# Kernel optimization log

Hardware: AMD Instinct MI355X
Metric: run time of the kernel (lower is better)

Reference implementation:

```python
import jax, jax.numpy as jnp
import numpy as np

# Model dims
B, S, D = 2, 1024, 1024          # batch, seq, d_model
NH, HD = 16, 64                  # n_heads, head_dim
E, K, H = 8, 2, 4096             # num_experts, experts_per_token, expert hidden
EPS = 1e-6
ROPE_BASE = 10000.0


def rmsnorm(x, w):
    # RMSNorm: x * rsqrt(mean(x^2) + eps) * weight (no mean-centering, no bias)
    return x * jax.lax.rsqrt(jnp.mean(x * x, axis=-1, keepdims=True) + EPS) * w


def apply_rope(q, k):
    # q,k: [B, NH, S, HD]; position_ids = arange(S) broadcast over batch
    hd = q.shape[-1]
    s = q.shape[2]
    inv_freq = 1.0 / (ROPE_BASE ** (jnp.arange(0, hd, 2, dtype=jnp.float32) / hd))
    freqs = jnp.arange(s, dtype=jnp.float32)[:, None] * inv_freq          # [S, HD/2]
    emb = jnp.concatenate([freqs, freqs], axis=-1)                        # [S, HD]
    cos = jnp.cos(emb)[None, None]                                        # [1,1,S,HD]
    sin = jnp.sin(emb)[None, None]

    def rotate_half(x):
        x1, x2 = jnp.split(x, 2, axis=-1)
        return jnp.concatenate([-x2, x1], axis=-1)

    return q * cos + rotate_half(q) * sin, k * cos + rotate_half(k) * sin


def setup_inputs() -> dict:
    key = jax.random.key(0)
    ks = jax.random.split(key, 9)
    sc = 0.02
    return {
        "x": jax.random.normal(ks[0], (B, S, D), jnp.float32),
        "attn_norm_w": jnp.ones((D,), jnp.float32),
        "wq": jax.random.normal(ks[1], (D, D), jnp.float32) * sc,
        "wk": jax.random.normal(ks[2], (D, D), jnp.float32) * sc,
        "wv": jax.random.normal(ks[3], (D, D), jnp.float32) * sc,
        "wo": jax.random.normal(ks[4], (D, D), jnp.float32) * sc,
        "moe_norm_w": jnp.ones((D,), jnp.float32),
        "gate_w": jax.random.normal(ks[5], (E, D), jnp.float32) * sc,
        "w1": jax.random.normal(ks[6], (E, H, D), jnp.float32) * sc,
        "b1": jnp.zeros((E, H), jnp.float32),
        "w2": jax.random.normal(ks[7], (E, D, H), jnp.float32) * sc,
        "b2": jnp.zeros((E, D), jnp.float32),
    }


def reference(x, attn_norm_w, wq, wk, wv, wo, moe_norm_w, gate_w, w1, b1, w2, b2):
    b, s, d = x.shape
    # --- pre-norm causal self-attention with RoPE (eval mode: no dropout) ---
    t = rmsnorm(x, attn_norm_w)
    q = (t @ wq.T).reshape(b, s, NH, HD).transpose(0, 2, 1, 3)
    k = (t @ wk.T).reshape(b, s, NH, HD).transpose(0, 2, 1, 3)
    v = (t @ wv.T).reshape(b, s, NH, HD).transpose(0, 2, 1, 3)
    q, k = apply_rope(q, k)
    scores = jnp.einsum("bhqd,bhkd->bhqk", q, k) / np.float32(np.sqrt(HD))
    causal = jnp.tril(jnp.ones((s, s), bool))
    scores = jnp.where(causal, scores, jnp.float32(-1e30))
    attn = jax.nn.softmax(scores, axis=-1)
    ao = jnp.einsum("bhqk,bhkd->bhqd", attn, v).transpose(0, 2, 1, 3).reshape(b, s, d)
    h = x + ao @ wo.T

    # --- sparse top-k MoE FFN (internal RMSNorm + residual) ---
    tn = rmsnorm(h, moe_norm_w).reshape(-1, d)                  # [T, D]
    logits = tn @ gate_w.T                                      # [T, E]
    gate_scores, idx = jax.lax.top_k(logits, K)                 # [T, K]
    rw = jax.nn.softmax(gate_scores, axis=-1)                   # [T, K]
    # compute all experts densely, then gather selected (same math as
    # gathering per-token expert weight matrices, far less memory traffic)
    hid = jax.nn.gelu(jnp.einsum("td,ehd->teh", tn, w1) + b1, approximate=False)
    eo = jnp.einsum("teh,edh->ted", hid, w2) + b2               # [T, E, D]
    sel = jnp.take_along_axis(eo, idx[:, :, None], axis=1)      # [T, K, D]
    moe_out = jnp.einsum("tkd,tk->td", sel, rw).reshape(b, s, d)
    return h + moe_out
```

## Files before the change

kernel.cpp:

```cpp
#include <hip/hip_runtime.h>
#include <hip/hip_bf16.h>
#include <hip/hip_fp16.h>


#define T_TOK 2048
#define DMODEL 1024
#define SEQ 1024
#define NEXP 8
#define HEXP 4096

typedef __attribute__((ext_vector_type(4))) float f32x4;
typedef __attribute__((ext_vector_type(4))) int i32x4;
typedef __attribute__((ext_vector_type(8))) short short8;
typedef __attribute__((ext_vector_type(8))) _Float16 half8;
typedef __attribute__((ext_vector_type(4))) _Float16 half4;

#define WAIT_VM3 asm volatile("s_waitcnt vmcnt(3)" ::: "memory")
#define WAIT_VM4 asm volatile("s_waitcnt vmcnt(4)" ::: "memory")
#define WAIT_VM6 asm volatile("s_waitcnt vmcnt(6)" ::: "memory")
#define WAIT_VM0 asm volatile("s_waitcnt vmcnt(0)" ::: "memory")
#define BARRIER __builtin_amdgcn_s_barrier()
#define SCHEDFENCE __builtin_amdgcn_sched_barrier(0)

__device__ __forceinline__ void gload16(const void* g, void* l)
{
    __builtin_amdgcn_global_load_lds((const __attribute__((address_space(1))) void*)g,
                                     (__attribute__((address_space(3))) void*)l, 16, 0, 0);
}

__device__ __forceinline__ void bsplit(float f, unsigned short& hi, unsigned short& lo)
{
    unsigned int u = __float_as_uint(f);
    unsigned int rh = (u + 0x7FFFu + ((u >> 16) & 1u)) >> 16;
    hi = (unsigned short)rh;
    float fl = f - __uint_as_float(rh << 16);
    unsigned int u2 = __float_as_uint(fl);
    lo = (unsigned short)((u2 + 0x7FFFu + ((u2 >> 16) & 1u)) >> 16);
}

__device__ __forceinline__ float gelu_fast(float v)
{
    float e = __expf(-1.5957691216f * v * (1.0f + 0.044715f * v * v));
    return v * __builtin_amdgcn_rcpf(1.0f + e);
}

__global__ __launch_bounds__(256) void cast2_f16_kernel(
    const float* __restrict__ s0, const float* __restrict__ s1,
    _Float16* __restrict__ d0, _Float16* __restrict__ d1, int n16)
{
    const float* src = blockIdx.y ? s1 : s0;
    _Float16* dst = blockIdx.y ? d1 : d0;
    int stride = gridDim.x * blockDim.x;
    for (int i = blockIdx.x * blockDim.x + threadIdx.x; i < n16; i += stride) {
        float4 a = ((const float4*)src)[4 * i];
        float4 b = ((const float4*)src)[4 * i + 1];
        float4 c = ((const float4*)src)[4 * i + 2];
        float4 d = ((const float4*)src)[4 * i + 3];
        half8 h0 = { (_Float16)a.x, (_Float16)a.y, (_Float16)a.z, (_Float16)a.w,
                     (_Float16)b.x, (_Float16)b.y, (_Float16)b.z, (_Float16)b.w };
        half8 h1 = { (_Float16)c.x, (_Float16)c.y, (_Float16)c.z, (_Float16)c.w,
                     (_Float16)d.x, (_Float16)d.y, (_Float16)d.z, (_Float16)d.w };
        *(half8*)(dst + (size_t)i * 16) = h0;
        *(half8*)(dst + (size_t)i * 16 + 8) = h1;
    }
}

__global__ __launch_bounds__(256) void split4_kernel(
    const float* __restrict__ s0, const float* __restrict__ s1,
    const float* __restrict__ s2, const float* __restrict__ s3,
    unsigned short* __restrict__ h0, unsigned short* __restrict__ h1,
    unsigned short* __restrict__ h2, unsigned short* __restrict__ h3,
    unsigned short* __restrict__ l0, unsigned short* __restrict__ l1,
    unsigned short* __restrict__ l2, unsigned short* __restrict__ l3, int n4)
{
    int z = blockIdx.y;
    const float* src = (z == 0) ? s0 : (z == 1) ? s1 : (z == 2) ? s2 : s3;
    unsigned short* hi = (z == 0) ? h0 : (z == 1) ? h1 : (z == 2) ? h2 : h3;
    unsigned short* lo = (z == 0) ? l0 : (z == 1) ? l1 : (z == 2) ? l2 : l3;
    int stride = gridDim.x * blockDim.x;
    for (int i = blockIdx.x * blockDim.x + threadIdx.x; i < n4; i += stride) {
        float4 v = ((const float4*)src)[i];
        ushort4 h, l;
        bsplit(v.x, h.x, l.x); bsplit(v.y, h.y, l.y);
        bsplit(v.z, h.z, l.z); bsplit(v.w, h.w, l.w);
        *(ushort4*)(hi + (size_t)i * 4) = h;
        *(ushort4*)(lo + (size_t)i * 4) = l;
    }
}

__global__ __launch_bounds__(256) void rmsnorm_kernel(const float* __restrict__ x,
                                                      const float* __restrict__ w,
                                                      float* __restrict__ of,
                                                      _Float16* __restrict__ oh,
                                                      unsigned short* __restrict__ ohi,
                                                      unsigned short* __restrict__ olo)
{
    int row = blockIdx.x;
    int t = threadIdx.x;
    float4 v = ((const float4*)(x + (size_t)row * DMODEL))[t];
    float ss = v.x * v.x + v.y * v.y + v.z * v.z + v.w * v.w;
#pragma unroll
    for (int off = 32; off > 0; off >>= 1) ss += __shfl_xor(ss, off);
    __shared__ float red[4];
    if ((t & 63) == 0) red[t >> 6] = ss;
    __syncthreads();
    float tot = red[0] + red[1] + red[2] + red[3];
    float sc = rsqrtf(tot * (1.0f / DMODEL) + 1e-6f);
    float4 w4 = ((const float4*)w)[t];
    float4 o;
    o.x = v.x * sc * w4.x; o.y = v.y * sc * w4.y; o.z = v.z * sc * w4.z; o.w = v.w * sc * w4.w;
    if (of) ((float4*)(of + (size_t)row * DMODEL))[t] = o;
    if (oh) {
        half4 h = { (_Float16)o.x, (_Float16)o.y, (_Float16)o.z, (_Float16)o.w };
        *(half4*)(oh + (size_t)row * DMODEL + t * 4) = h;
    }
    if (ohi) {
        ushort4 h, l;
        bsplit(o.x, h.x, l.x); bsplit(o.y, h.y, l.y);
        bsplit(o.z, h.z, l.z); bsplit(o.w, h.w, l.w);
        *(ushort4*)(ohi + (size_t)row * DMODEL + t * 4) = h;
        *(ushort4*)(olo + (size_t)row * DMODEL + t * 4) = l;
    }
}

__global__ __launch_bounds__(256) void gemm_split_kernel(
    const unsigned short* __restrict__ aH, const unsigned short* __restrict__ aL,
    const unsigned short* __restrict__ b0H, const unsigned short* __restrict__ b0L,
    const unsigned short* __restrict__ b1H, const unsigned short* __restrict__ b1L,
    const unsigned short* __restrict__ b2H, const unsigned short* __restrict__ b2L,
    float* __restrict__ C0, float* __restrict__ C1, float* __restrict__ C2,
    const float* __restrict__ resid, int K)
{
    const unsigned short* bH = (blockIdx.z == 0) ? b0H : (blockIdx.z == 1 ? b1H : b2H);
    const unsigned short* bL = (blockIdx.z == 0) ? b0L : (blockIdx.z == 1 ? b1L : b2L);
    float* C = (blockIdx.z == 0) ? C0 : (blockIdx.z == 1 ? C1 : C2);
    int m0 = blockIdx.y * 128, n0 = blockIdx.x * 64;
    __shared__ unsigned short AsH[2][128 * 32];
    __shared__ unsigned short AsL[2][128 * 32];
    __shared__ unsigned short BsH[2][64 * 32];
    __shared__ unsigned short BsL[2][64 * 32];
    int t = threadIdx.x, w = t >> 6, l = t & 63;
    int sa = l >> 2, sc = (l & 3) * 8;
    const unsigned short* gAH0 = aH + (size_t)(m0 + w * 32 + sa) * K + sc;
    const unsigned short* gAH1 = aH + (size_t)(m0 + w * 32 + 16 + sa) * K + sc;
    const unsigned short* gAL0 = aL + (size_t)(m0 + w * 32 + sa) * K + sc;
    const unsigned short* gAL1 = aL + (size_t)(m0 + w * 32 + 16 + sa) * K + sc;
    const unsigned short* gBH0 = bH + (size_t)(n0 + w * 16 + sa) * K + sc;
    const unsigned short* gBL0 = bL + (size_t)(n0 + w * 16 + sa) * K + sc;
    const int aoff0 = (w * 32) * 32;
    const int aoff1 = (w * 32 + 16) * 32;
    const int boff0 = (w * 16) * 32;
    int wr = w >> 1, wc = w & 1;
    f32x4 zero = { 0.0f, 0.0f, 0.0f, 0.0f };
    f32x4 acc[4][2];
#pragma unroll
    for (int i = 0; i < 4; i++)
#pragma unroll
        for (int j = 0; j < 2; j++) acc[i][j] = zero;

#define GS_STAGE(B, K0) do { \
    gload16(gAH0 + (K0), &AsH[B][aoff0]); gload16(gAH1 + (K0), &AsH[B][aoff1]); \
    gload16(gAL0 + (K0), &AsL[B][aoff0]); gload16(gAL1 + (K0), &AsL[B][aoff1]); \
    gload16(gBH0 + (K0), &BsH[B][boff0]); gload16(gBL0 + (K0), &BsL[B][boff0]); \
} while (0)

#define GS_COMPUTE(B) do { \
    short8 ah[4], al[4], bh8[2], bl8[2]; \
    _Pragma("unroll") \
    for (int mi = 0; mi < 4; mi++) { \
        int base = (wr * 64 + mi * 16 + (l & 15)) * 32 + (l >> 4) * 8; \
        ah[mi] = *(const short8*)&AsH[B][base]; \
        al[mi] = *(const short8*)&AsL[B][base]; } \
    _Pragma("unroll") \
    for (int ni = 0; ni < 2; ni++) { \
        int base = (wc * 32 + ni * 16 + (l & 15)) * 32 + (l >> 4) * 8; \
        bh8[ni] = *(const short8*)&BsH[B][base]; \
        bl8[ni] = *(const short8*)&BsL[B][base]; } \
    _Pragma("unroll") \
    for (int mi = 0; mi < 4; mi++) \
        _Pragma("unroll") \
        for (int ni = 0; ni < 2; ni++) { \
            acc[mi][ni] = __builtin_amdgcn_mfma_f32_16x16x32_bf16(ah[mi], bh8[ni], acc[mi][ni], 0, 0, 0); \
            acc[mi][ni] = __builtin_amdgcn_mfma_f32_16x16x32_bf16(ah[mi], bl8[ni], acc[mi][ni], 0, 0, 0); \
            acc[mi][ni] = __builtin_amdgcn_mfma_f32_16x16x32_bf16(al[mi], bh8[ni], acc[mi][ni], 0, 0, 0); } \
} while (0)

    const int nt = K >> 5;
    GS_STAGE(0, 0);
    for (int kt = 0; kt < nt; kt += 2) {
        GS_STAGE(1, (kt + 1) << 5);
        WAIT_VM6;
        BARRIER; SCHEDFENCE;
        GS_COMPUTE(0);
        BARRIER;
        if (kt + 2 < nt) {
            GS_STAGE(0, (kt + 2) << 5);
            WAIT_VM6;
        } else {
            WAIT_VM0;
        }
        BARRIER; SCHEDFENCE;
        GS_COMPUTE(1);
        BARRIER;
    }
#undef GS_STAGE
#undef GS_COMPUTE

#pragma unroll
    for (int mi = 0; mi < 4; mi++) {
#pragma unroll
        for (int r = 0; r < 4; r++) {
            int row = m0 + wr * 64 + mi * 16 + (l >> 4) * 4 + r;
#pragma unroll
            for (int ni = 0; ni < 2; ni++) {
                int col = n0 + wc * 32 + ni * 16 + (l & 15);
                float v = acc[mi][ni][r];
                if (resid) v += resid[(size_t)row * DMODEL + col];
                C[(size_t)row * DMODEL + col] = v;
            }
        }
    }
}

__global__ __launch_bounds__(256) void rope_split_kernel(
    const float* __restrict__ qf, const float* __restrict__ kf,
    unsigned short* __restrict__ qHi, unsigned short* __restrict__ qLo,
    unsigned short* __restrict__ kHi, unsigned short* __restrict__ kLo)
{
    int i = blockIdx.x * 256 + threadIdx.x;
    int tok = i >> 9;
    int r = i & 511;
    int hh = r >> 5, ii = r & 31;
    int s = tok & (SEQ - 1);
    int b = tok >> 10;
    float invf = powf(10000.0f, -(float)(2 * ii) * (1.0f / 64.0f));
    float ang = (float)s * invf;
    float c = cosf(ang), sn = sinf(ang);
    size_t base = (size_t)tok * DMODEL + hh * 64 + ii;
    float q1 = qf[base], q2 = qf[base + 32];
    float k1 = kf[base], k2 = kf[base + 32];
    float rq1 = (q1 * c - q2 * sn) * 0.125f;
    float rq2 = (q2 * c + q1 * sn) * 0.125f;
    float rk1 = k1 * c - k2 * sn;
    float rk2 = k2 * c + k1 * sn;
    int bh = b * 16 + hh;
    size_t qb = ((size_t)bh * SEQ + s) * 64 + ii;
    unsigned short h, lo;
    bsplit(rq1, h, lo); qHi[qb] = h; qLo[qb] = lo;
    bsplit(rq2, h, lo); qHi[qb + 32] = h; qLo[qb + 32] = lo;
    size_t kb = (size_t)bh * (SEQ * 64) + (size_t)(s >> 6) * 4096 + (size_t)(s & 63) * 64;
    int d1 = ii, d2 = ii + 32;
    int p1 = (((d1 >> 3) ^ (s & 7)) << 3) | (d1 & 7);
    int p2 = (((d2 >> 3) ^ (s & 7)) << 3) | (d2 & 7);
    bsplit(rk1, h, lo); kHi[kb + p1] = h; kLo[kb + p1] = lo;
    bsplit(rk2, h, lo); kHi[kb + p2] = h; kLo[kb + p2] = lo;
}

__global__ __launch_bounds__(256) void vtrans_kernel(const float* __restrict__ vf,
                                                     unsigned short* __restrict__ vtHi,
                                                     unsigned short* __restrict__ vtLo)
{
    int sb = blockIdx.x, bh = blockIdx.y;
    int b = bh >> 4, h = bh & 15;
    __shared__ unsigned short tH[64][72];
    __shared__ unsigned short tL[64][72];
    int t = threadIdx.x;
#pragma unroll
    for (int i = 0; i < 4; i++) {
        int idx = i * 256 + t, row = idx >> 4, c4 = idx & 15;
        float4 v = *(const float4*)(vf + (size_t)(b * SEQ + sb * 64 + row) * DMODEL + h * 64 + c4 * 4);
        unsigned short hh, ll;
        bsplit(v.x, hh, ll); tH[c4 * 4 + 0][row] = hh; tL[c4 * 4 + 0][row] = ll;
        bsplit(v.y, hh, ll); tH[c4 * 4 + 1][row] = hh; tL[c4 * 4 + 1][row] = ll;
        bsplit(v.z, hh, ll); tH[c4 * 4 + 2][row] = hh; tL[c4 * 4 + 2][row] = ll;
        bsplit(v.w, hh, ll); tH[c4 * 4 + 3][row] = hh; tL[c4 * 4 + 3][row] = ll;
    }
    __syncthreads();
#pragma unroll
    for (int i = 0; i < 4; i++) {
        int idx = i * 256 + t, d = idx >> 4, sc4 = idx & 15;
        ushort4 oh = { tH[d][sc4 * 4 + 0], tH[d][sc4 * 4 + 1], tH[d][sc4 * 4 + 2], tH[d][sc4 * 4 + 3] };
        ushort4 ol = { tL[d][sc4 * 4 + 0], tL[d][sc4 * 4 + 1], tL[d][sc4 * 4 + 2], tL[d][sc4 * 4 + 3] };
        size_t off = (size_t)bh * (64 * SEQ) + (size_t)sb * 4096 + (size_t)d * 64
                   + (((sc4 >> 1) ^ (d & 7)) << 3) + ((sc4 & 1) << 2);
        *(ushort4*)(vtHi + off) = oh;
        *(ushort4*)(vtLo + off) = ol;
    }
}

__global__ __launch_bounds__(512) void attn_mfma_kernel(
    const unsigned short* __restrict__ qHi, const unsigned short* __restrict__ qLo,
    const unsigned short* __restrict__ kHi, const unsigned short* __restrict__ kLo,
    const unsigned short* __restrict__ vtHi, const unsigned short* __restrict__ vtLo,
    float* __restrict__ Opart, float* __restrict__ mscr, float* __restrict__ lscr)
{
    int qt = 7 - blockIdx.x;
    int bh = blockIdx.y, ks = blockIdx.z;
    int t = threadIdx.x, w = t >> 6, l = t & 63;
    int lq = l & 15, g = l >> 4, lx = lq & 7;
    __shared__ unsigned short KsH[2][4096];
    __shared__ unsigned short KsL[2][4096];
    __shared__ unsigned short VsH[2][4096];
    __shared__ unsigned short VsL[2][4096];
    __shared__ unsigned short PsH[8][1024];
    __shared__ unsigned short PsL[8][1024];
    const size_t hb = (size_t)bh * (SEQ * 64);
    const unsigned short* kHp = kHi + hb;
    const unsigned short* kLp = kLo + hb;
    const unsigned short* vHp = vtHi + hb;
    const unsigned short* vLp = vtLo + hb;
    int qrow = qt * 128 + w * 16 + lq;
    short8 qh[2], qlo8[2];
#pragma unroll
    for (int c = 0; c < 2; c++) {
        size_t off = hb + (size_t)qrow * 64 + c * 32 + g * 8;
        qh[c]   = *(const short8*)(qHi + off);
        qlo8[c] = *(const short8*)(qLo + off);
    }
    f32x4 zero = { 0.0f, 0.0f, 0.0f, 0.0f };
    f32x4 acc_o[4];
#pragma unroll
    for (int i = 0; i < 4; i++) acc_o[i] = zero;
    float mrun = -3.0e38f, lrun = 0.0f;
    int ktl = ks ? (qt + 1) : 0;
    int kth = ks ? (2 * qt + 2) : (qt + 1);

#define AT_STAGE(B, KT) do { \
    size_t so = (size_t)(KT) * 4096 + (w * 64 + l) * 8; \
    gload16(kHp + so, &KsH[B][w * 512]); \
    gload16(kLp + so, &KsL[B][w * 512]); \
    gload16(vHp + so, &VsH[B][w * 512]); \
    gload16(vLp + so, &VsL[B][w * 512]); \
} while (0)

#define AT_COMPUTE(B, KT) do { \
    f32x4 sacc[4]; \
    _Pragma("unroll") \
    for (int i = 0; i < 4; i++) sacc[i] = zero; \
    _Pragma("unroll") \
    for (int nf = 0; nf < 4; nf++) { \
        _Pragma("unroll") \
        for (int c = 0; c < 2; c++) { \
            int ka = (nf * 16 + lq) * 64 + (((c * 4 + g) ^ lx) << 3); \
            short8 kh = *(const short8*)&KsH[B][ka]; \
            short8 kl = *(const short8*)&KsL[B][ka]; \
            sacc[nf] = __builtin_amdgcn_mfma_f32_16x16x32_bf16(kh, qh[c], sacc[nf], 0, 0, 0); \
            sacc[nf] = __builtin_amdgcn_mfma_f32_16x16x32_bf16(kh, qlo8[c], sacc[nf], 0, 0, 0); \
            sacc[nf] = __builtin_amdgcn_mfma_f32_16x16x32_bf16(kl, qh[c], sacc[nf], 0, 0, 0); \
        } \
    } \
    _Pragma("unroll") \
    for (int nf = 0; nf < 4; nf++) \
        _Pragma("unroll") \
        for (int r = 0; r < 4; r++) \
            if ((KT) * 64 + nf * 16 + g * 4 + r > qrow) sacc[nf][r] = -1.0e30f; \
    float mt = sacc[0][0]; \
    _Pragma("unroll") \
    for (int nf = 0; nf < 4; nf++) \
        _Pragma("unroll") \
        for (int r = 0; r < 4; r++) mt = fmaxf(mt, sacc[nf][r]); \
    mt = fmaxf(mt, __shfl_xor(mt, 16)); \
    mt = fmaxf(mt, __shfl_xor(mt, 32)); \
    float mnew = fmaxf(mrun, mt); \
    float p[4][4]; \
    float ps = 0.0f; \
    _Pragma("unroll") \
    for (int nf = 0; nf < 4; nf++) \
        _Pragma("unroll") \
        for (int r = 0; r < 4; r++) { \
            float e = __expf(sacc[nf][r] - mnew); \
            p[nf][r] = e; \
            ps += e; \
        } \
    ps += __shfl_xor(ps, 16); \
    ps += __shfl_xor(ps, 32); \
    float scale = __expf(mrun - mnew); \
    lrun = lrun * scale + ps; \
    mrun = mnew; \
    _Pragma("unroll") \
    for (int nf = 0; nf < 4; nf++) { \
        ushort4 ph, pl; \
        bsplit(p[nf][0], ph.x, pl.x); bsplit(p[nf][1], ph.y, pl.y); \
        bsplit(p[nf][2], ph.z, pl.z); bsplit(p[nf][3], ph.w, pl.w); \
        int pa = lq * 64 + (((nf * 2 + (g >> 1)) ^ lx) << 3) + ((g & 1) << 2); \
        *(ushort4*)&PsH[w][pa] = ph; \
        *(ushort4*)&PsL[w][pa] = pl; \
    } \
    float scq[4]; \
    _Pragma("unroll") \
    for (int r = 0; r < 4; r++) scq[r] = __shfl(scale, g * 4 + r); \
    _Pragma("unroll") \
    for (int df = 0; df < 4; df++) \
        _Pragma("unroll") \
        for (int r = 0; r < 4; r++) acc_o[df][r] *= scq[r]; \
    _Pragma("unroll") \
    for (int c = 0; c < 2; c++) { \
        int pa = lq * 64 + (((c * 4 + g) ^ lx) << 3); \
        short8 ph8 = *(const short8*)&PsH[w][pa]; \
        short8 pl8 = *(const short8*)&PsL[w][pa]; \
        _Pragma("unroll") \
        for (int df = 0; df < 4; df++) { \
            int va = (df * 16 + lq) * 64 + (((c * 4 + g) ^ lx) << 3); \
            short8 vh = *(const short8*)&VsH[B][va]; \
            short8 vl = *(const short8*)&VsL[B][va]; \
            acc_o[df] = __builtin_amdgcn_mfma_f32_16x16x32_bf16(ph8, vh, acc_o[df], 0, 0, 0); \
            acc_o[df] = __builtin_amdgcn_mfma_f32_16x16x32_bf16(ph8, vl, acc_o[df], 0, 0, 0); \
            acc_o[df] = __builtin_amdgcn_mfma_f32_16x16x32_bf16(pl8, vh, acc_o[df], 0, 0, 0); \
        } \
    } \
} while (0)

    int kt = ktl;
    AT_STAGE(0, kt);
    for (; kt + 1 < kth; kt += 2) {
        AT_STAGE(1, kt + 1);
        WAIT_VM4;
        BARRIER; SCHEDFENCE;
        AT_COMPUTE(0, kt);
        BARRIER;
        if (kt + 2 < kth) {
            AT_STAGE(0, kt + 2);
            WAIT_VM4;
        } else {
            WAIT_VM0;
        }
        BARRIER; SCHEDFENCE;
        AT_COMPUTE(1, kt + 1);
        BARRIER;
    }
    if (kt < kth) {
        WAIT_VM0;
        BARRIER; SCHEDFENCE;
        AT_COMPUTE(0, kt);
    }
#undef AT_STAGE
#undef AT_COMPUTE

    if (g == 0) {
        size_t mi = (size_t)(ks * 32 + bh) * SEQ + (size_t)(qt * 128 + w * 16 + lq);
        mscr[mi] = mrun;
        lscr[mi] = lrun;
    }
#pragma unroll
    for (int df = 0; df < 4; df++)
#pragma unroll
        for (int r = 0; r < 4; r++) {
            size_t row = (size_t)(ks * 32 + bh) * SEQ + (size_t)(qt * 128 + w * 16 + g * 4 + r);
            Opart[row * 64 + df * 16 + lq] = acc_o[df][r];
        }
}

__global__ __launch_bounds__(256) void attn_combine_kernel(
    const float* __restrict__ Opart, const float* __restrict__ mscr,
    const float* __restrict__ lscr,
    unsigned short* __restrict__ aoHi, unsigned short* __restrict__ aoLo)
{
    int i = blockIdx.x * 256 + threadIdx.x;
    int d4 = i & 15;
    int qr = (i >> 4) & (SEQ - 1);
    int bh = i >> 14;
    int b = bh >> 4, h = bh & 15;
    size_t r0 = (size_t)bh * SEQ + qr;
    size_t r1 = (size_t)(32 + bh) * SEQ + qr;
    float m0 = mscr[r0], m1 = mscr[r1];
    float l0 = lscr[r0], l1 = lscr[r1];
    float m = fmaxf(m0, m1);
    float w0 = __expf(m0 - m), w1 = __expf(m1 - m);
    float dn = 1.0f / (w0 * l0 + w1 * l1);
    float4 o0 = *(const float4*)(Opart + r0 * 64 + d4 * 4);
    float4 o1 = *(const float4*)(Opart + r1 * 64 + d4 * 4);
    float4 o;
    o.x = (w0 * o0.x + w1 * o1.x) * dn;
    o.y = (w0 * o0.y + w1 * o1.y) * dn;
    o.z = (w0 * o0.z + w1 * o1.z) * dn;
    o.w = (w0 * o0.w + w1 * o1.w) * dn;
    ushort4 hs, ls;
    bsplit(o.x, hs.x, ls.x); bsplit(o.y, hs.y, ls.y);
    bsplit(o.z, hs.z, ls.z); bsplit(o.w, hs.w, ls.w);
    size_t base = (size_t)b * SEQ * DMODEL + (size_t)qr * DMODEL + h * 64 + d4 * 4;
    *(ushort4*)(aoHi + base) = hs;
    *(ushort4*)(aoLo + base) = ls;
}

__global__ __launch_bounds__(256) void gate_kernel(const float* __restrict__ tn2f,
                                                   const float* __restrict__ gw,
                                                   float* __restrict__ logits)
{
    int tok = blockIdx.x;
    int t = threadIdx.x, e = t >> 5, l32 = t & 31;
    const float* xr = tn2f + (size_t)tok * DMODEL;
    const float* gr = gw + (size_t)e * DMODEL;
    float s = 0.0f;
    for (int j = l32; j < DMODEL; j += 32) s += xr[j] * gr[j];
#pragma unroll
    for (int off = 16; off > 0; off >>= 1) s += __shfl_down(s, off, 32);
    if (l32 == 0) logits[tok * NEXP + e] = s;
}

__global__ void zero_kernel(int* p, int n)
{
    int i = blockIdx.x * blockDim.x + threadIdx.x;
    if (i < n) p[i] = 0;
}

__global__ void top2_kernel(const float* __restrict__ logits, float* __restrict__ rw,
                            int* __restrict__ cnt, int* __restrict__ entry)
{
    int t = blockIdx.x * blockDim.x + threadIdx.x;
    if (t >= T_TOK) return;
    float l[8];
#pragma unroll
    for (int e = 0; e < 8; e++) l[e] = logits[t * 8 + e];
    int e0 = 0;
#pragma unroll
    for (int e = 1; e < 8; e++) if (l[e] > l[e0]) e0 = e;
    int e1 = (e0 == 0) ? 1 : 0;
#pragma unroll
    for (int e = 0; e < 8; e++) if (e != e0 && l[e] > l[e1]) e1 = e;
    float ex = expf(l[e1] - l[e0]);
    float denom = 1.0f + ex;
    rw[t * 2 + 0] = 1.0f / denom;
    rw[t * 2 + 1] = ex / denom;
    int pos = atomicAdd(&cnt[e0], 1);
    entry[e0 * 2048 + pos] = t * 2;
    pos = atomicAdd(&cnt[e1], 1);
    entry[e1 * 2048 + pos] = t * 2 + 1;
}

__global__ void offs_kernel(const int* __restrict__ cnt, int* __restrict__ offs)
{
    if (threadIdx.x == 0) {
        int s = 0;
        for (int e = 0; e < 8; e++) { offs[e] = s; s += cnt[e]; }
    }
}

__global__ __launch_bounds__(256) void moe_gemm1_kernel(
    const _Float16* __restrict__ tn2h, const _Float16* __restrict__ w1h,
    const float* __restrict__ b1, const int* __restrict__ cnt, const int* __restrict__ offs,
    const int* __restrict__ entry, _Float16* __restrict__ hid)
{
    int bid = blockIdx.x;
    int e = bid & 7;
    int n_i = (bid >> 3) & 31;
    int m_i = bid >> 8;
    int ne = cnt[e];
    int m0 = m_i * 128;
    if (m0 >= ne) return;
    int n0 = n_i * 128;
    __shared__ _Float16 As[2][128 * 32];
    __shared__ _Float16 Bs[2][128 * 32];
    int t = threadIdx.x, w = t >> 6, l = t & 63;
    int sa = l >> 2, sc = (l & 3) * 8;
    int g0 = entry[e * 2048 + min(m0 + w * 32 + sa, ne - 1)] >> 1;
    int g1 = entry[e * 2048 + min(m0 + w * 32 + 16 + sa, ne - 1)] >> 1;
    const _Float16* gA0 = tn2h + (size_t)g0 * DMODEL + sc;
    const _Float16* gA1 = tn2h + (size_t)g1 * DMODEL + sc;
    const _Float16* w1e = w1h + (size_t)e * HEXP * DMODEL;
    const _Float16* gB0 = w1e + (size_t)(n0 + w * 32 + sa) * DMODEL + sc;
    const _Float16* gB1 = w1e + (size_t)(n0 + w * 32 + 16 + sa) * DMODEL + sc;
    const int aoff0 = (w * 32) * 32, aoff1 = (w * 32 + 16) * 32;
    int wr = w >> 1, wc = w & 1;
    f32x4 zero = { 0.0f, 0.0f, 0.0f, 0.0f };
    f32x4 acc[4][4];
#pragma unroll
    for (int i = 0; i < 4; i++)
#pragma unroll
        for (int j = 0; j < 4; j++) acc[i][j] = zero;

#define M1_STAGE(B, K0) do { \
    gload16(gA0 + (K0), &As[B][aoff0]); gload16(gA1 + (K0), &As[B][aoff1]); \
    gload16(gB0 + (K0), &Bs[B][aoff0]); gload16(gB1 + (K0), &Bs[B][aoff1]); \
} while (0)

#define M1_COMPUTE(B) do { \
    half8 af[4], bfr[4]; \
    _Pragma("unroll") \
    for (int mi = 0; mi < 4; mi++) \
        af[mi] = *(const half8*)&As[B][(wr * 64 + mi * 16 + (l & 15)) * 32 + (l >> 4) * 8]; \
    _Pragma("unroll") \
    for (int ni = 0; ni < 4; ni++) \
        bfr[ni] = *(const half8*)&Bs[B][(wc * 64 + ni * 16 + (l & 15)) * 32 + (l >> 4) * 8]; \
    _Pragma("unroll") \
    for (int mi = 0; mi < 4; mi++) \
        _Pragma("unroll") \
        for (int ni = 0; ni < 4; ni++) \
            acc[mi][ni] = __builtin_amdgcn_mfma_f32_16x16x32_f16(af[mi], bfr[ni], acc[mi][ni], 0, 0, 0); \
} while (0)

    const int nt = DMODEL >> 5;
    M1_STAGE(0, 0);
    for (int kt = 0; kt < nt; kt += 2) {
        M1_STAGE(1, (kt + 1) << 5);
        WAIT_VM4;
        BARRIER; SCHEDFENCE;
        M1_COMPUTE(0);
        BARRIER;
        if (kt + 2 < nt) {
            M1_STAGE(0, (kt + 2) << 5);
            WAIT_VM4;
        } else {
            WAIT_VM0;
        }
        BARRIER; SCHEDFENCE;
        M1_COMPUTE(1);
        BARRIER;
    }
#undef M1_STAGE
#undef M1_COMPUTE

    int off_e = offs[e];
#pragma unroll
    for (int mi = 0; mi < 4; mi++) {
#pragma unroll
        for (int r = 0; r < 4; r++) {
            int row = m0 + wr * 64 + mi * 16 + (l >> 4) * 4 + r;
            if (row < ne) {
                size_t orow = (size_t)(off_e + row) * HEXP;
#pragma unroll
                for (int ni = 0; ni < 4; ni++) {
                    int cg = n0 + wc * 64 + ni * 16 + (l & 15);
                    float v = acc[mi][ni][r] + b1[e * HEXP + cg];
                    hid[orow + cg] = (_Float16)gelu_fast(v);
                }
            }
        }
    }
}

__global__ __launch_bounds__(512) void moe_gemm2_kernel(
    const _Float16* __restrict__ hid, const _Float16* __restrict__ w2h,
    const float* __restrict__ b2, const int* __restrict__ cnt, const int* __restrict__ offs,
    const int* __restrict__ entry,
    float* __restrict__ eoA, float* __restrict__ eoB,
    float* __restrict__ eoC, float* __restrict__ eoD)
{
    int bid = blockIdx.x;
    int e = bid & 7;
    int rest = bid >> 3;
    int n_i = rest & 7;
    int rest2 = rest >> 3;
    int ks = rest2 & 3;
    int m_i = rest2 >> 2;
    int ne = cnt[e];
    int m0 = m_i * 256;
    if (m0 >= ne) return;
    int n0 = n_i * 128;
    int kbase = ks * (HEXP / 4);
    float* eoP = (ks == 0) ? eoA : (ks == 1) ? eoB : (ks == 2) ? eoC : eoD;
    __shared__ _Float16 As[2][256 * 32];
    __shared__ _Float16 Bs[2][128 * 32];
    int t = threadIdx.x, w = t >> 6, l = t & 63;
    int off_e = offs[e];
    int sa = l >> 2, sc = (l & 3) * 8;
    int r0 = off_e + min(m0 + w * 32 + sa, ne - 1);
    int r1 = off_e + min(m0 + w * 32 + 16 + sa, ne - 1);
    const _Float16* gA0 = hid + (size_t)r0 * HEXP + kbase + sc;
    const _Float16* gA1 = hid + (size_t)r1 * HEXP + kbase + sc;
    const _Float16* w2e = w2h + (size_t)e * DMODEL * HEXP;
    const _Float16* gB0 = w2e + (size_t)(n0 + w * 16 + sa) * HEXP + kbase + sc;
    const int aoff0 = (w * 32) * 32, aoff1 = (w * 32 + 16) * 32;
    const int boff0 = (w * 16) * 32;
    int wr = w >> 1, wc = w & 1;
    f32x4 zero = { 0.0f, 0.0f, 0.0f, 0.0f };
    f32x4 acc[4][4];
#pragma unroll
    for (int i = 0; i < 4; i++)
#pragma unroll
        for (int j = 0; j < 4; j++) acc[i][j] = zero;

#define M2_STAGE(B, K0) do { \
    gload16(gA0 + (K0), &As[B][aoff0]); gload16(gA1 + (K0), &As[B][aoff1]); \
    gload16(gB0 + (K0), &Bs[B][boff0]); \
} while (0)

#define M2_COMPUTE(B) do { \
    half8 af[4], bfr[4]; \
    _Pragma("unroll") \
    for (int mi = 0; mi < 4; mi++) \
        af[mi] = *(const half8*)&As[B][(wr * 64 + mi * 16 + (l & 15)) * 32 + (l >> 4) * 8]; \
    _Pragma("unroll") \
    for (int ni = 0; ni < 4; ni++) \
        bfr[ni] = *(const half8*)&Bs[B][(wc * 64 + ni * 16 + (l & 15)) * 32 + (l >> 4) * 8]; \
    _Pragma("unroll") \
    for (int mi = 0; mi < 4; mi++) \
        _Pragma("unroll") \
        for (int ni = 0; ni < 4; ni++) \
            acc[mi][ni] = __builtin_amdgcn_mfma_f32_16x16x32_f16(af[mi], bfr[ni], acc[mi][ni], 0, 0, 0); \
} while (0)

    const int nt = (HEXP / 4) >> 5;
    M2_STAGE(0, 0);
    for (int kt = 0; kt < nt; kt += 2) {
        M2_STAGE(1, (kt + 1) << 5);
        WAIT_VM3;
        BARRIER; SCHEDFENCE;
        M2_COMPUTE(0);
        BARRIER;
        if (kt + 2 < nt) {
            M2_STAGE(0, (kt + 2) << 5);
            WAIT_VM3;
        } else {
            WAIT_VM0;
        }
        BARRIER; SCHEDFENCE;
        M2_COMPUTE(1);
        BARRIER;
    }
#undef M2_STAGE
#undef M2_COMPUTE

#pragma unroll
    for (int mi = 0; mi < 4; mi++) {
#pragma unroll
        for (int r = 0; r < 4; r++) {
            int row = m0 + wr * 64 + mi * 16 + (l >> 4) * 4 + r;
            if (row < ne) {
                int t2k = entry[e * 2048 + row];
#pragma unroll
                for (int ni = 0; ni < 4; ni++) {
                    int cg = n0 + wc * 64 + ni * 16 + (l & 15);
                    float v = acc[mi][ni][r];
                    if (ks == 0) v += b2[e * DMODEL + cg];
                    eoP[(size_t)t2k * DMODEL + cg] = v;
                }
            }
        }
    }
}

__global__ __launch_bounds__(256) void combine_kernel(const float* __restrict__ hf,
                                                      const float* __restrict__ eoA,
                                                      const float* __restrict__ eoB,
                                                      const float* __restrict__ eoC,
                                                      const float* __restrict__ eoD,
                                                      const float* __restrict__ rw,
                                                      float* __restrict__ out)
{
    int i = blockIdx.x * 256 + threadIdx.x;
    int tok = i >> 8;
    int d4 = i & 255;
    float4 hv = ((const float4*)hf)[i];
    float p0 = rw[tok * 2], p1 = rw[tok * 2 + 1];
    size_t i0 = (size_t)(tok * 2) * 256 + d4;
    size_t i1 = (size_t)(tok * 2 + 1) * 256 + d4;
    float4 a0 = ((const float4*)eoA)[i0];
    float4 b0 = ((const float4*)eoB)[i0];
    float4 c0 = ((const float4*)eoC)[i0];
    float4 d0 = ((const float4*)eoD)[i0];
    float4 a1 = ((const float4*)eoA)[i1];
    float4 b1 = ((const float4*)eoB)[i1];
    float4 c1 = ((const float4*)eoC)[i1];
    float4 d1 = ((const float4*)eoD)[i1];
    float4 o;
    o.x = hv.x + p0 * (a0.x + b0.x + c0.x + d0.x) + p1 * (a1.x + b1.x + c1.x + d1.x);
    o.y = hv.y + p0 * (a0.y + b0.y + c0.y + d0.y) + p1 * (a1.y + b1.y + c1.y + d1.y);
    o.z = hv.z + p0 * (a0.z + b0.z + c0.z + d0.z) + p1 * (a1.z + b1.z + c1.z + d1.z);
    o.w = hv.w + p0 * (a0.w + b0.w + c0.w + d0.w) + p1 * (a1.w + b1.w + c1.w + d1.w);
    ((float4*)out)[i] = o;
}

extern "C" void kernel_launch(void* const* d_in, const int* in_sizes, int n_in,
                              void* d_out, int out_size, void* d_ws, size_t ws_size,
                              hipStream_t stream)
{
    const float* x   = (const float*)d_in[0];
    const float* anw = (const float*)d_in[1];
    const float* wq  = (const float*)d_in[2];
    const float* wk  = (const float*)d_in[3];
    const float* wv  = (const float*)d_in[4];
    const float* wo  = (const float*)d_in[5];
    const float* mnw = (const float*)d_in[6];
    const float* gw  = (const float*)d_in[7];
    const float* w1  = (const float*)d_in[8];
    const float* b1  = (const float*)d_in[9];
    const float* w2  = (const float*)d_in[10];
    const float* b2  = (const float*)d_in[11];
    float* out = (float*)d_out;

    char* p = (char*)d_ws;
    auto alloc = [&](size_t bytes) { char* q = p; p += (bytes + 255) & ~(size_t)255; return q; };
    const size_t TD = (size_t)T_TOK * DMODEL;
    unsigned short* tnHi = (unsigned short*)alloc(TD * 2);
    unsigned short* tnLo = (unsigned short*)alloc(TD * 2);
    float*    qf   = (float*)alloc(TD * 4);
    float*    kf   = (float*)alloc(TD * 4);
    float*    vf   = (float*)alloc(TD * 4);
    unsigned short* qHi = (unsigned short*)alloc(TD * 2);
    unsigned short* qLo = (unsigned short*)alloc(TD * 2);
    unsigned short* kHi = (unsigned short*)alloc(TD * 2);
    unsigned short* kLo = (unsigned short*)alloc(TD * 2);
    float*    hf   = (float*)alloc(TD * 4);
    unsigned short* wqH = (unsigned short*)alloc((size_t)DMODEL * DMODEL * 2);
    unsigned short* wqL = (unsigned short*)alloc((size_t)DMODEL * DMODEL * 2);
    unsigned short* wkH = (unsigned short*)alloc((size_t)DMODEL * DMODEL * 2);
    unsigned short* wkL = (unsigned short*)alloc((size_t)DMODEL * DMODEL * 2);
    unsigned short* wvH = (unsigned short*)alloc((size_t)DMODEL * DMODEL * 2);
    unsigned short* wvL = (unsigned short*)alloc((size_t)DMODEL * DMODEL * 2);
    unsigned short* woH = (unsigned short*)alloc((size_t)DMODEL * DMODEL * 2);
    unsigned short* woL = (unsigned short*)alloc((size_t)DMODEL * DMODEL * 2);
    _Float16* w1h  = (_Float16*)alloc((size_t)NEXP * HEXP * DMODEL * 2);
    _Float16* w2h  = (_Float16*)alloc((size_t)NEXP * HEXP * DMODEL * 2);
    _Float16* hid  = (_Float16*)alloc((size_t)4096 * HEXP * 2);
    float*    logits = (float*)alloc((size_t)T_TOK * NEXP * 4);
    float*    rw   = (float*)alloc((size_t)T_TOK * 2 * 4);
    int*      cnt  = (int*)alloc(256);
    int*      offs = (int*)alloc(256);
    int*      entry = (int*)alloc((size_t)NEXP * 2048 * 4);
    float*    mscr = (float*)alloc((size_t)2 * 32 * SEQ * 4);
    float*    lscr = (float*)alloc((size_t)2 * 32 * SEQ * 4);
    (void)ws_size; (void)in_sizes; (void)n_in; (void)out_size;

    unsigned short* vtHi = (unsigned short*)qf;
    unsigned short* vtLo = (unsigned short*)qf + TD;
    float* tn2f = qf;
    unsigned short* aoHi = (unsigned short*)kf;
    unsigned short* aoLo = (unsigned short*)kf + TD;
    _Float16* tn2h = (_Float16*)vf;
    float* eoA = (float*)qHi;
    float* eoB = (float*)wqH;
    float* Opart = (float*)w1h;
    float* eoC = (float*)((char*)w1h + (size_t)32 * 1024 * 1024);
    float* eoD = (float*)((char*)w1h + (size_t)48 * 1024 * 1024);

    split4_kernel<<<dim3(512, 4), 256, 0, stream>>>(wq, wk, wv, wo,
        wqH, wkH, wvH, woH, wqL, wkL, wvL, woL, DMODEL * DMODEL / 4);

    rmsnorm_kernel<<<T_TOK, 256, 0, stream>>>(x, anw, nullptr, (_Float16*)nullptr, tnHi, tnLo);
    gemm_split_kernel<<<dim3(16, 16, 3), 256, 0, stream>>>(
        tnHi, tnLo, wqH, wqL, wkH, wkL, wvH, wvL, qf, kf, vf, nullptr, DMODEL);
    rope_split_kernel<<<4096, 256, 0, stream>>>(qf, kf, qHi, qLo, kHi, kLo);
    vtrans_kernel<<<dim3(16, 32), 256, 0, stream>>>(vf, vtHi, vtLo);
    attn_mfma_kernel<<<dim3(8, 32, 2), 512, 0, stream>>>(qHi, qLo, kHi, kLo, vtHi, vtLo,
                                                         Opart, mscr, lscr);
    attn_combine_kernel<<<2048, 256, 0, stream>>>(Opart, mscr, lscr, aoHi, aoLo);
    gemm_split_kernel<<<dim3(16, 16, 1), 256, 0, stream>>>(
        aoHi, aoLo, woH, woL, woH, woL, woH, woL, hf, hf, hf, x, DMODEL);

    cast2_f16_kernel<<<dim3(4096, 2), 256, 0, stream>>>(w1, w2, w1h, w2h,
                                                        NEXP * HEXP * DMODEL / 16);

    rmsnorm_kernel<<<T_TOK, 256, 0, stream>>>(hf, mnw, tn2f, tn2h, nullptr, nullptr);
    gate_kernel<<<T_TOK, 256, 0, stream>>>(tn2f, gw, logits);
    zero_kernel<<<1, 64, 0, stream>>>(cnt, 8);
    top2_kernel<<<8, 256, 0, stream>>>(logits, rw, cnt, entry);
    offs_kernel<<<1, 1, 0, stream>>>(cnt, offs);
    moe_gemm1_kernel<<<4096, 256, 0, stream>>>(tn2h, w1h, b1, cnt, offs, entry, hid);
    moe_gemm2_kernel<<<2048, 512, 0, stream>>>(hid, w2h, b2, cnt, offs, entry,
                                               eoA, eoB, eoC, eoD);
    combine_kernel<<<2048, 256, 0, stream>>>(hf, eoA, eoB, eoC, eoD, rw, out);
}
```

Measured before the change: 422.4 us.

## Fuse fp32-to-fp16 expert weight cast into MoE GEMM B-tile staging

Removes the separate cast kernel that converted all w1/w2 expert weights to fp16 before the MoE GEMMs. Both GEMMs now read fp32 weight rows into registers one k-step ahead, convert them to fp16 and write them to LDS themselves; only the token operand keeps the async global-to-LDS path. This drops a full pass over the weights plus the fp16 copy write and its buffers. In exchange, each M-tile reads twice as many weight bytes, the B loads go through registers instead of direct-to-LDS, and the stage now waits on LDS writes.

```diff
diff --git a/kernel.cpp b/kernel.cpp
--- a/kernel.cpp
+++ b/kernel.cpp
@@ -19,6 +19,7 @@
 #define WAIT_VM4 asm volatile("s_waitcnt vmcnt(4)" ::: "memory")
 #define WAIT_VM6 asm volatile("s_waitcnt vmcnt(6)" ::: "memory")
 #define WAIT_VM0 asm volatile("s_waitcnt vmcnt(0)" ::: "memory")
+#define WAIT_LGKM0 asm volatile("s_waitcnt lgkmcnt(0)" ::: "memory")
 #define BARRIER __builtin_amdgcn_s_barrier()
 #define SCHEDFENCE __builtin_amdgcn_sched_barrier(0)
 
@@ -42,27 +43,6 @@
 {
     float e = __expf(-1.5957691216f * v * (1.0f + 0.044715f * v * v));
     return v * __builtin_amdgcn_rcpf(1.0f + e);
-}
-
-__global__ __launch_bounds__(256) void cast2_f16_kernel(
-    const float* __restrict__ s0, const float* __restrict__ s1,
-    _Float16* __restrict__ d0, _Float16* __restrict__ d1, int n16)
-{
-    const float* src = blockIdx.y ? s1 : s0;
-    _Float16* dst = blockIdx.y ? d1 : d0;
-    int stride = gridDim.x * blockDim.x;
-    for (int i = blockIdx.x * blockDim.x + threadIdx.x; i < n16; i += stride) {
-        float4 a = ((const float4*)src)[4 * i];
-        float4 b = ((const float4*)src)[4 * i + 1];
-        float4 c = ((const float4*)src)[4 * i + 2];
-        float4 d = ((const float4*)src)[4 * i + 3];
-        half8 h0 = { (_Float16)a.x, (_Float16)a.y, (_Float16)a.z, (_Float16)a.w,
-                     (_Float16)b.x, (_Float16)b.y, (_Float16)b.z, (_Float16)b.w };
-        half8 h1 = { (_Float16)c.x, (_Float16)c.y, (_Float16)c.z, (_Float16)c.w,
-                     (_Float16)d.x, (_Float16)d.y, (_Float16)d.z, (_Float16)d.w };
-        *(half8*)(dst + (size_t)i * 16) = h0;
-        *(half8*)(dst + (size_t)i * 16 + 8) = h1;
-    }
 }
 
 __global__ __launch_bounds__(256) void split4_kernel(
@@ -536,7 +516,7 @@
 }
 
 __global__ __launch_bounds__(256) void moe_gemm1_kernel(
-    const _Float16* __restrict__ tn2h, const _Float16* __restrict__ w1h,
+    const _Float16* __restrict__ tn2h, const float* __restrict__ w1f,
     const float* __restrict__ b1, const int* __restrict__ cnt, const int* __restrict__ offs,
     const int* __restrict__ entry, _Float16* __restrict__ hid)
 {
@@ -556,10 +536,12 @@
     int g1 = entry[e * 2048 + min(m0 + w * 32 + 16 + sa, ne - 1)] >> 1;
     const _Float16* gA0 = tn2h + (size_t)g0 * DMODEL + sc;
     const _Float16* gA1 = tn2h + (size_t)g1 * DMODEL + sc;
-    const _Float16* w1e = w1h + (size_t)e * HEXP * DMODEL;
-    const _Float16* gB0 = w1e + (size_t)(n0 + w * 32 + sa) * DMODEL + sc;
-    const _Float16* gB1 = w1e + (size_t)(n0 + w * 32 + 16 + sa) * DMODEL + sc;
+    const float* w1e = w1f + (size_t)e * HEXP * DMODEL;
+    const float* gB0f = w1e + (size_t)(n0 + w * 32 + sa) * DMODEL + sc;
+    const float* gB1f = w1e + (size_t)(n0 + w * 32 + 16 + sa) * DMODEL + sc;
     const int aoff0 = (w * 32) * 32, aoff1 = (w * 32 + 16) * 32;
+    const int boff0 = (w * 32 + sa) * 32 + sc;
+    const int boff1 = (w * 32 + 16 + sa) * 32 + sc;
     int wr = w >> 1, wc = w & 1;
     f32x4 zero = { 0.0f, 0.0f, 0.0f, 0.0f };
     f32x4 acc[4][4];
@@ -567,10 +549,24 @@
     for (int i = 0; i < 4; i++)
 #pragma unroll
         for (int j = 0; j < 4; j++) acc[i][j] = zero;
+    f32x4 br0, br1, br2, br3;
+
+#define M1_LOADB(K0) do { \
+    br0 = *(const f32x4*)(gB0f + (K0)); \
+    br1 = *(const f32x4*)(gB0f + (K0) + 4); \
+    br2 = *(const f32x4*)(gB1f + (K0)); \
+    br3 = *(const f32x4*)(gB1f + (K0) + 4); \
+} while (0)
 
 #define M1_STAGE(B, K0) do { \
+    half8 hb0 = { (_Float16)br0[0], (_Float16)br0[1], (_Float16)br0[2], (_Float16)br0[3], \
+                  (_Float16)br1[0], (_Float16)br1[1], (_Float16)br1[2], (_Float16)br1[3] }; \
+    half8 hb1 = { (_Float16)br2[0], (_Float16)br2[1], (_Float16)br2[2], (_Float16)br2[3], \
+                  (_Float16)br3[0], (_Float16)br3[1], (_Float16)br3[2], (_Float16)br3[3] }; \
+    *(half8*)&Bs[B][boff0] = hb0; \
+    *(half8*)&Bs[B][boff1] = hb1; \
     gload16(gA0 + (K0), &As[B][aoff0]); gload16(gA1 + (K0), &As[B][aoff1]); \
-    gload16(gB0 + (K0), &Bs[B][aoff0]); gload16(gB1 + (K0), &Bs[B][aoff1]); \
+    WAIT_LGKM0; \
 } while (0)
 
 #define M1_COMPUTE(B) do { \
@@ -589,16 +585,20 @@
 } while (0)
 
     const int nt = DMODEL >> 5;
+    M1_LOADB(0);
     M1_STAGE(0, 0);
+    M1_LOADB(32);
     for (int kt = 0; kt < nt; kt += 2) {
         M1_STAGE(1, (kt + 1) << 5);
-        WAIT_VM4;
+        if (kt + 2 < nt) M1_LOADB((kt + 2) << 5);
+        WAIT_VM6;
         BARRIER; SCHEDFENCE;
         M1_COMPUTE(0);
         BARRIER;
         if (kt + 2 < nt) {
             M1_STAGE(0, (kt + 2) << 5);
-            WAIT_VM4;
+            if (kt + 3 < nt) M1_LOADB((kt + 3) << 5);
+            WAIT_VM6;
         } else {
             WAIT_VM0;
         }
@@ -606,6 +606,7 @@
         M1_COMPUTE(1);
         BARRIER;
     }
+#undef M1_LOADB
 #undef M1_STAGE
 #undef M1_COMPUTE
 
@@ -629,7 +630,7 @@
 }
 
 __global__ __launch_bounds__(512) void moe_gemm2_kernel(
-    const _Float16* __restrict__ hid, const _Float16* __restrict__ w2h,
+    const _Float16* __restrict__ hid, const float* __restrict__ w2f,
     const float* __restrict__ b2, const int* __restrict__ cnt, const int* __restrict__ offs,
     const int* __restrict__ entry,
     float* __restrict__ eoA, float* __restrict__ eoB,
@@ -657,10 +658,10 @@
     int r1 = off_e + min(m0 + w * 32 + 16 + sa, ne - 1);
     const _Float16* gA0 = hid + (size_t)r0 * HEXP + kbase + sc;
     const _Float16* gA1 = hid + (size_t)r1 * HEXP + kbase + sc;
-    const _Float16* w2e = w2h + (size_t)e * DMODEL * HEXP;
-    const _Float16* gB0 = w2e + (size_t)(n0 + w * 16 + sa) * HEXP + kbase + sc;
+    const float* w2e = w2f + (size_t)e * DMODEL * HEXP;
+    const float* gB0f = w2e + (size_t)(n0 + w * 16 + sa) * HEXP + kbase + sc;
     const int aoff0 = (w * 32) * 32, aoff1 = (w * 32 + 16) * 32;
-    const int boff0 = (w * 16) * 32;
+    const int boff0 = (w * 16 + sa) * 32 + sc;
     int wr = w >> 1, wc = w & 1;
     f32x4 zero = { 0.0f, 0.0f, 0.0f, 0.0f };
     f32x4 acc[4][4];
@@ -668,10 +669,19 @@
     for (int i = 0; i < 4; i++)
 #pragma unroll
         for (int j = 0; j < 4; j++) acc[i][j] = zero;
+    f32x4 br0, br1;
+
+#define M2_LOADB(K0) do { \
+    br0 = *(const f32x4*)(gB0f + (K0)); \
+    br1 = *(const f32x4*)(gB0f + (K0) + 4); \
+} while (0)
 
 #define M2_STAGE(B, K0) do { \
+    half8 hb0 = { (_Float16)br0[0], (_Float16)br0[1], (_Float16)br0[2], (_Float16)br0[3], \
+                  (_Float16)br1[0], (_Float16)br1[1], (_Float16)br1[2], (_Float16)br1[3] }; \
+    *(half8*)&Bs[B][boff0] = hb0; \
     gload16(gA0 + (K0), &As[B][aoff0]); gload16(gA1 + (K0), &As[B][aoff1]); \
-    gload16(gB0 + (K0), &Bs[B][boff0]); \
+    WAIT_LGKM0; \
 } while (0)
 
 #define M2_COMPUTE(B) do { \
@@ -690,16 +700,20 @@
 } while (0)
 
     const int nt = (HEXP / 4) >> 5;
+    M2_LOADB(0);
     M2_STAGE(0, 0);
+    M2_LOADB(32);
     for (int kt = 0; kt < nt; kt += 2) {
         M2_STAGE(1, (kt + 1) << 5);
-        WAIT_VM3;
+        if (kt + 2 < nt) M2_LOADB((kt + 2) << 5);
+        WAIT_VM4;
         BARRIER; SCHEDFENCE;
         M2_COMPUTE(0);
         BARRIER;
         if (kt + 2 < nt) {
             M2_STAGE(0, (kt + 2) << 5);
-            WAIT_VM3;
+            if (kt + 3 < nt) M2_LOADB((kt + 3) << 5);
+            WAIT_VM4;
         } else {
             WAIT_VM0;
         }
@@ -707,6 +721,7 @@
         M2_COMPUTE(1);
         BARRIER;
     }
+#undef M2_LOADB
 #undef M2_STAGE
 #undef M2_COMPUTE
 
@@ -799,8 +814,7 @@
     unsigned short* wvL = (unsigned short*)alloc((size_t)DMODEL * DMODEL * 2);
     unsigned short* woH = (unsigned short*)alloc((size_t)DMODEL * DMODEL * 2);
     unsigned short* woL = (unsigned short*)alloc((size_t)DMODEL * DMODEL * 2);
-    _Float16* w1h  = (_Float16*)alloc((size_t)NEXP * HEXP * DMODEL * 2);
-    _Float16* w2h  = (_Float16*)alloc((size_t)NEXP * HEXP * DMODEL * 2);
+    char*     moescr = alloc((size_t)64 * 1024 * 1024);
     _Float16* hid  = (_Float16*)alloc((size_t)4096 * HEXP * 2);
     float*    logits = (float*)alloc((size_t)T_TOK * NEXP * 4);
     float*    rw   = (float*)alloc((size_t)T_TOK * 2 * 4);
@@ -819,9 +833,9 @@
     _Float16* tn2h = (_Float16*)vf;
     float* eoA = (float*)qHi;
     float* eoB = (float*)wqH;
-    float* Opart = (float*)w1h;
-    float* eoC = (float*)((char*)w1h + (size_t)32 * 1024 * 1024);
-    float* eoD = (float*)((char*)w1h + (size_t)48 * 1024 * 1024);
+    float* Opart = (float*)moescr;
+    float* eoC = (float*)(moescr + (size_t)32 * 1024 * 1024);
+    float* eoD = (float*)(moescr + (size_t)48 * 1024 * 1024);
 
     split4_kernel<<<dim3(512, 4), 256, 0, stream>>>(wq, wk, wv, wo,
         wqH, wkH, wvH, woH, wqL, wkL, wvL, woL, DMODEL * DMODEL / 4);
@@ -837,16 +851,13 @@
     gemm_split_kernel<<<dim3(16, 16, 1), 256, 0, stream>>>(
         aoHi, aoLo, woH, woL, woH, woL, woH, woL, hf, hf, hf, x, DMODEL);
 
-    cast2_f16_kernel<<<dim3(4096, 2), 256, 0, stream>>>(w1, w2, w1h, w2h,
-                                                        NEXP * HEXP * DMODEL / 16);
-
     rmsnorm_kernel<<<T_TOK, 256, 0, stream>>>(hf, mnw, tn2f, tn2h, nullptr, nullptr);
     gate_kernel<<<T_TOK, 256, 0, stream>>>(tn2f, gw, logits);
     zero_kernel<<<1, 64, 0, stream>>>(cnt, 8);
     top2_kernel<<<8, 256, 0, stream>>>(logits, rw, cnt, entry);
     offs_kernel<<<1, 1, 0, stream>>>(cnt, offs);
-    moe_gemm1_kernel<<<4096, 256, 0, stream>>>(tn2h, w1h, b1, cnt, offs, entry, hid);
-    moe_gemm2_kernel<<<2048, 512, 0, stream>>>(hid, w2h, b2, cnt, offs, entry,
+    moe_gemm1_kernel<<<4096, 256, 0, stream>>>(tn2h, w1, b1, cnt, offs, entry, hid);
+    moe_gemm2_kernel<<<2048, 512, 0, stream>>>(hid, w2, b2, cnt, offs, entry,
                                                eoA, eoB, eoC, eoD);
     combine_kernel<<<2048, 256, 0, stream>>>(hf, eoA, eoB, eoC, eoD, rw, out);
 }
```

Result: no change. 419.2 us (-0.8%).
